# Optimization experiments

Measured on AMD Instinct MI355X. Metric: run time of the kernel, lower is better.

Reference implementation:

```python
import jax, jax.numpy as jnp
import numpy as np

N = 4096      # nodes
D = 256       # input_dim
OUT = 256     # output_dim
K = 4         # num_kernels
TOPK = 16
CHEB_T = 2
ROW_TEMP = 1.0
EPS = 1e-9


def setup_inputs() -> dict:
    key = jax.random.key(0)
    ks = jax.random.split(key, 6)
    X = jax.random.normal(ks[0], (N, D), dtype=jnp.float32)
    L_k = jax.random.normal(ks[1], (K, D, D), dtype=jnp.float32) * 0.02
    alpha = jnp.ones((K,), dtype=jnp.float32)
    theta = jax.random.normal(ks[2], (CHEB_T + 1, D), dtype=jnp.float32) * 0.02
    rho_raw = jnp.zeros((), dtype=jnp.float32)
    proj_w = jax.random.normal(ks[3], (OUT, D), dtype=jnp.float32) / np.float32(np.sqrt(D))
    proj_b = jnp.zeros((OUT,), dtype=jnp.float32)
    v0 = jax.random.normal(ks[4], (N, 1), dtype=jnp.float32)  # power-iteration init
    return dict(X=X, L_k=L_k, alpha=alpha, theta=theta, rho_raw=rho_raw,
                proj_w=proj_w, proj_b=proj_b, v0=v0)


def reference(X, L_k, alpha, theta, rho_raw, proj_w, proj_b, v0):
    n, d = X.shape
    k = L_k.shape[0]
    # 1) kernel stack: A_k = X L_k X^T / sqrt(D), row softmax  -> (K,N,N)
    A = jnp.einsum('nd,kde,me->knm', X, L_k, X) / jnp.sqrt(jnp.float32(d))
    H_stack = jax.nn.softmax(A / max(ROW_TEMP, 1e-6), axis=-1)
    w = jax.nn.softmax(alpha)[:, None, None]
    H_fused = (H_stack * w).sum(0)                               # (N,N)
    # 2) soft incidence via per-row top-k + renormalize, scattered into B (N, K*N)
    vals, idx = jax.lax.top_k(H_stack, TOPK)                     # (K,N,TOPK)
    vals = vals / (vals.sum(-1, keepdims=True) + EPS)
    E = k * n
    cols = jnp.arange(k)[:, None, None] * n + jnp.arange(n)[None, :, None]
    cols = jnp.broadcast_to(cols, idx.shape)
    B = jnp.zeros((n, E), X.dtype).at[idx.reshape(-1), cols.reshape(-1)].set(vals.reshape(-1))
    W = jnp.ones((E,), X.dtype)
    # 3) hypergraph Laplacian L = I - Dv^{-1/2} B W De^{-1} B^T Dv^{-1/2}
    De = B.sum(0) + EPS
    Dv = (B * W[None, :]).sum(1) + EPS
    Dv_is = 1.0 / jnp.sqrt(Dv)
    S = (B * (W / De)[None, :]) @ B.T                            # (N,N)
    S_norm = Dv_is[:, None] * S * Dv_is[None, :]
    L = jnp.eye(n, dtype=X.dtype) - S_norm
    # 4) lambda_max via power iteration on detached L (constant, as in torch)
    Ld = jax.lax.stop_gradient(L)
    v = v0 / (jnp.linalg.norm(v0) + EPS)
    for _ in range(5):
        v = Ld @ v
        v = v / (jnp.linalg.norm(v) + EPS)
    lam = jnp.maximum((v.T @ (Ld @ v)).squeeze(), jnp.float32(1e-3))
    lam = jax.lax.stop_gradient(lam)
    # Chebyshev filter
    L_tilde = (2.0 / lam) * L - jnp.eye(n, dtype=X.dtype)
    out = X * theta[0][None, :]
    T0 = X
    T1 = L_tilde @ X
    out = out + T1 * theta[1][None, :]
    for t in range(2, CHEB_T + 1):
        T2 = 2.0 * (L_tilde @ T1) - T0
        out = out + T2 * theta[t][None, :]
        T0, T1 = T1, T2
    Z_spec = jax.nn.elu(out)
    # 5) residual blend with kernel diffusion
    Z_kern = H_fused @ X
    rho = jax.nn.sigmoid(rho_raw)
    Z_mix = rho * Z_spec + (1.0 - rho) * Z_kern
    # 6) final projection
    return Z_mix @ proj_w.T + proj_b[None, :]
```

## Files before the change

kernel.cpp:

```cpp
#include <hip/hip_runtime.h>
#include <math.h>

#define N_ 4096
#define D_ 256
#define K_ 4
#define TK_ 16
#define E_ (K_ * N_)
#define NENT_ (E_ * TK_)

typedef unsigned short u16;
typedef unsigned int u32;
typedef __attribute__((ext_vector_type(8))) short bf16x8;
typedef __attribute__((ext_vector_type(4))) float f32x4;

__device__ __forceinline__ u16 bf16_rne(float x) {
  u32 u = __float_as_uint(x);
  u32 r = u + 0x7FFFu + ((u >> 16) & 1u);
  return (u16)(r >> 16);
}


__global__ void scalars_kernel(const float* __restrict__ alpha,
                               const float* __restrict__ rho_raw,
                               float* __restrict__ scal) {
  if (threadIdx.x == 0) {
    float m = alpha[0];
    for (int k = 1; k < K_; ++k) m = fmaxf(m, alpha[k]);
    float e[K_]; float s = 0.f;
    for (int k = 0; k < K_; ++k) { e[k] = expf(alpha[k] - m); s += e[k]; }
    for (int k = 0; k < K_; ++k) scal[k] = e[k] / s;
    scal[4] = 1.0f / (1.0f + expf(-rho_raw[0]));
  }
}

__global__ void dvis_kernel(const float* __restrict__ DvAcc, float* __restrict__ Dvis) {
  int i = blockIdx.x * 256 + threadIdx.x;
  Dvis[i] = 1.0f / sqrtf(DvAcc[i] + 1e-9f);
}

__global__ void make_tkvd(const float* __restrict__ tkv, const int* __restrict__ tki,
                          const float* __restrict__ Dvis, float* __restrict__ tkvd) {
  int i = blockIdx.x * 256 + threadIdx.x;
  tkvd[i] = tkv[i] * Dvis[tki[i]];
}

__global__ void cvt_split4(const float* __restrict__ in, u16* __restrict__ hi,
                           u16* __restrict__ lo) {
  int i = (blockIdx.x * 256 + threadIdx.x) * 4;
  float4 v = *(const float4*)(in + i);
  u16 h0 = bf16_rne(v.x), h1 = bf16_rne(v.y), h2 = bf16_rne(v.z), h3 = bf16_rne(v.w);
  float f0 = __uint_as_float((u32)h0 << 16), f1 = __uint_as_float((u32)h1 << 16);
  float f2 = __uint_as_float((u32)h2 << 16), f3 = __uint_as_float((u32)h3 << 16);
  u16 l0 = bf16_rne(v.x - f0), l1 = bf16_rne(v.y - f1);
  u16 l2 = bf16_rne(v.z - f2), l3 = bf16_rne(v.w - f3);
  *(uint2*)(hi + i) = make_uint2((u32)h0 | ((u32)h1 << 16), (u32)h2 | ((u32)h3 << 16));
  *(uint2*)(lo + i) = make_uint2((u32)l0 | ((u32)l1 << 16), (u32)l2 | ((u32)l3 << 16));
}

__global__ __launch_bounds__(256) void transpose_split(const float* __restrict__ X,
                                                       u16* __restrict__ ht,
                                                       u16* __restrict__ lt) {
  __shared__ float tile[32][33];
  const int tx = threadIdx.x & 31, ty = threadIdx.x >> 5;
  const int d0 = blockIdx.x * 32, n0 = blockIdx.y * 32;
#pragma unroll
  for (int q = 0; q < 4; ++q)
    tile[ty + q * 8][tx] = X[(size_t)(n0 + ty + q * 8) * D_ + d0 + tx];
  __syncthreads();
#pragma unroll
  for (int q = 0; q < 4; ++q) {
    int dd = ty + q * 8;
    float v = tile[tx][dd];
    u16 h = bf16_rne(v);
    float hf = __uint_as_float((u32)h << 16);
    u16 l = bf16_rne(v - hf);
    ht[(size_t)(d0 + dd) * N_ + n0 + tx] = h;
    lt[(size_t)(d0 + dd) * N_ + n0 + tx] = l;
  }
}

__global__ __launch_bounds__(256) void gemm_nn64_split(const float* __restrict__ A,
                                                       const float* __restrict__ B,
                                                       u16* __restrict__ Ch,
                                                       u16* __restrict__ Cl,
                                                       int Kdim, int lda, int ldb, int ldc) {
  __shared__ float As[16][68];
  __shared__ float Bs[16][68];
  const int tid = threadIdx.x;
  const int bm = blockIdx.x * 64, bn = blockIdx.y * 64;
  const int lrA = tid >> 2, lcA = (tid & 3) * 4;
  const int rrB = tid >> 4, ccB = (tid & 15) * 4;
  const int tx = tid & 15, ty = tid >> 4;
  const float* Ap = A + (size_t)(bm + lrA) * lda + lcA;
  const float* Bp = B + (size_t)rrB * ldb + bn + ccB;
  float acc[4][4] = {};
  for (int k0 = 0; k0 < Kdim; k0 += 16) {
    float4 av = *(const float4*)(Ap + k0);
    float4 bv = *(const float4*)(Bp + (size_t)k0 * ldb);
    __syncthreads();
    As[lcA + 0][lrA] = av.x; As[lcA + 1][lrA] = av.y;
    As[lcA + 2][lrA] = av.z; As[lcA + 3][lrA] = av.w;
    *(float4*)&Bs[rrB][ccB] = bv;
    __syncthreads();
#pragma unroll
    for (int kk = 0; kk < 16; ++kk) {
      float a[4], b[4];
      *(float4*)a = *(const float4*)&As[kk][ty * 4];
      *(float4*)b = *(const float4*)&Bs[kk][tx * 4];
#pragma unroll
      for (int i = 0; i < 4; ++i)
#pragma unroll
        for (int j = 0; j < 4; ++j) acc[i][j] += a[i] * b[j];
    }
  }
#pragma unroll
  for (int i = 0; i < 4; ++i) {
    int row = bm + ty * 4 + i;
    u16 h[4], lo[4];
#pragma unroll
    for (int j = 0; j < 4; ++j) {
      h[j] = bf16_rne(acc[i][j]);
      lo[j] = bf16_rne(acc[i][j] - __uint_as_float((u32)h[j] << 16));
    }
    size_t base = (size_t)row * ldc + bn + tx * 4;
    *(uint2*)(Ch + base) = make_uint2((u32)h[0] | ((u32)h[1] << 16), (u32)h[2] | ((u32)h[3] << 16));
    *(uint2*)(Cl + base) = make_uint2((u32)lo[0] | ((u32)lo[1] << 16), (u32)lo[2] | ((u32)lo[3] << 16));
  }
}

__global__ __launch_bounds__(256) void gemm_nt64_bias(const float* __restrict__ A,
                                                      const float* __restrict__ B,
                                                      const float* __restrict__ bias,
                                                      float* __restrict__ C,
                                                      int Kdim, int lda, int ldb, int ldc) {
  __shared__ float As[16][68];
  __shared__ float Bs[16][68];
  const int tid = threadIdx.x;
  const int bm = blockIdx.x * 64, bn = blockIdx.y * 64;
  const int lr = tid >> 2, lc = (tid & 3) * 4;
  const int tx = tid & 15, ty = tid >> 4;
  const float* Ap = A + (size_t)(bm + lr) * lda + lc;
  const float* Bp = B + (size_t)(bn + lr) * ldb + lc;
  float acc[4][4] = {};
  for (int k0 = 0; k0 < Kdim; k0 += 16) {
    float4 av = *(const float4*)(Ap + k0);
    float4 bv = *(const float4*)(Bp + k0);
    __syncthreads();
    As[lc + 0][lr] = av.x; As[lc + 1][lr] = av.y; As[lc + 2][lr] = av.z; As[lc + 3][lr] = av.w;
    Bs[lc + 0][lr] = bv.x; Bs[lc + 1][lr] = bv.y; Bs[lc + 2][lr] = bv.z; Bs[lc + 3][lr] = bv.w;
    __syncthreads();
#pragma unroll
    for (int kk = 0; kk < 16; ++kk) {
      float a[4], b[4];
      *(float4*)a = *(const float4*)&As[kk][ty * 4];
      *(float4*)b = *(const float4*)&Bs[kk][tx * 4];
#pragma unroll
      for (int i = 0; i < 4; ++i)
#pragma unroll
        for (int j = 0; j < 4; ++j) acc[i][j] += a[i] * b[j];
    }
  }
#pragma unroll
  for (int i = 0; i < 4; ++i) {
    int row = bm + ty * 4 + i;
    float4 o;
    o.x = acc[i][0] + bias[bn + tx * 4 + 0];
    o.y = acc[i][1] + bias[bn + tx * 4 + 1];
    o.z = acc[i][2] + bias[bn + tx * 4 + 2];
    o.w = acc[i][3] + bias[bn + tx * 4 + 3];
    *(float4*)(C + (size_t)row * ldc + bn + tx * 4) = o;
  }
}


__global__ __launch_bounds__(256) void scores_mfma(const u16* __restrict__ Ahg,
                                                   const u16* __restrict__ Alg,
                                                   const u16* __restrict__ Bhg,
                                                   const u16* __restrict__ Blg,
                                                   float* __restrict__ C, float scale) {
  __shared__ char smem[65536];
  const int tid = threadIdx.x;
  const int bm = blockIdx.x * 128, bn = blockIdx.y * 128;
  const int w = tid >> 6, l = tid & 63;
  const int wr = (w >> 1) * 64, wc = (w & 1) * 64;
  const int srow = tid >> 3, scol = (tid & 7) * 8;
  const int lb = l & 15, lke = (l >> 4) * 8;
  const u16* bh0 = Bhg + (size_t)(bn + wc + 0  + lb) * D_ + lke;
  const u16* bh1 = Bhg + (size_t)(bn + wc + 16 + lb) * D_ + lke;
  const u16* bh2 = Bhg + (size_t)(bn + wc + 32 + lb) * D_ + lke;
  const u16* bh3 = Bhg + (size_t)(bn + wc + 48 + lb) * D_ + lke;
  const size_t dlo = (size_t)(Blg - Bhg);
  const int aoff[4] = {
    (srow + 0)  * 128 + ((scol * 2) ^ (((srow + 0)  & 7) << 4)),
    (srow + 32) * 128 + ((scol * 2) ^ (((srow + 32) & 7) << 4)),
    (srow + 64) * 128 + ((scol * 2) ^ (((srow + 64) & 7) << 4)),
    (srow + 96) * 128 + ((scol * 2) ^ (((srow + 96) & 7) << 4)) };
  f32x4 acc[4][4];
#pragma unroll
  for (int i = 0; i < 4; ++i)
#pragma unroll
    for (int j = 0; j < 4; ++j) { acc[i][j][0] = 0.f; acc[i][j][1] = 0.f; acc[i][j][2] = 0.f; acc[i][j][3] = 0.f; }

  uint4 ah[4], al[4];
#pragma unroll
  for (int ii = 0; ii < 4; ++ii) {
    int r = srow + ii * 32;
    ah[ii] = *(const uint4*)(Ahg + (size_t)(bm + r) * D_ + scol);
    al[ii] = *(const uint4*)(Alg + (size_t)(bm + r) * D_ + scol);
  }
  {
    char* bAh = smem; char* bAl = smem + 16384;
#pragma unroll
    for (int ii = 0; ii < 4; ++ii) {
      *(uint4*)(bAh + aoff[ii]) = ah[ii];
      *(uint4*)(bAl + aoff[ii]) = al[ii];
    }
  }
  __syncthreads();

  for (int c = 0; c < 4; ++c) {
    char* bAh = smem + ((c & 1) << 15);
    char* bAl = bAh + 16384;
    const bool hn = (c < 3);
    if (hn) {
      const int kn = (c + 1) * 64;
#pragma unroll
      for (int ii = 0; ii < 4; ++ii) {
        int r = srow + ii * 32;
        ah[ii] = *(const uint4*)(Ahg + (size_t)(bm + r) * D_ + kn + scol);
        al[ii] = *(const uint4*)(Alg + (size_t)(bm + r) * D_ + kn + scol);
      }
    }
#pragma unroll
    for (int kk = 0; kk < 2; ++kk) {
      const int kb = kk * 64 + ((l >> 4) << 4);
      const int ge = c * 64 + kk * 32;
      bf16x8 fbh[4], fbl[4];
      fbh[0] = *(const bf16x8*)(bh0 + ge); fbl[0] = *(const bf16x8*)(bh0 + dlo + ge);
      fbh[1] = *(const bf16x8*)(bh1 + ge); fbl[1] = *(const bf16x8*)(bh1 + dlo + ge);
      fbh[2] = *(const bf16x8*)(bh2 + ge); fbl[2] = *(const bf16x8*)(bh2 + dlo + ge);
      fbh[3] = *(const bf16x8*)(bh3 + ge); fbl[3] = *(const bf16x8*)(bh3 + dlo + ge);
#pragma unroll
      for (int i = 0; i < 4; ++i) {
        int ra = wr + i * 16 + lb;
        int oa = ra * 128 + (kb ^ ((ra & 7) << 4));
        bf16x8 fah = *(const bf16x8*)(bAh + oa);
        bf16x8 fal = *(const bf16x8*)(bAl + oa);
#pragma unroll
        for (int j = 0; j < 4; ++j) {
          acc[i][j] = __builtin_amdgcn_mfma_f32_16x16x32_bf16(fah, fbh[j], acc[i][j], 0, 0, 0);
          acc[i][j] = __builtin_amdgcn_mfma_f32_16x16x32_bf16(fah, fbl[j], acc[i][j], 0, 0, 0);
          acc[i][j] = __builtin_amdgcn_mfma_f32_16x16x32_bf16(fal, fbh[j], acc[i][j], 0, 0, 0);
        }
      }
    }
    if (hn) {
      char* nAh = smem + (((c + 1) & 1) << 15);
      char* nAl = nAh + 16384;
#pragma unroll
      for (int ii = 0; ii < 4; ++ii) {
        *(uint4*)(nAh + aoff[ii]) = ah[ii];
        *(uint4*)(nAl + aoff[ii]) = al[ii];
      }
    }
    __syncthreads();
  }
  float* Cs = (float*)smem;
  const int cr = (l >> 4) * 4, cc = l & 15;
#pragma unroll
  for (int p = 0; p < 2; ++p) {
    __syncthreads();
    if ((w >> 1) == p) {
#pragma unroll
      for (int i = 0; i < 4; ++i)
#pragma unroll
        for (int r = 0; r < 4; ++r) {
          int rl = i * 16 + cr + r;
          int sw = ((rl >> 2) & 3) << 4;
#pragma unroll
          for (int j = 0; j < 4; ++j) {
            int cl = wc + j * 16 + cc;
            Cs[rl * 128 + (cl ^ sw)] = acc[i][j][r] * scale;
          }
        }
    }
    __syncthreads();
#pragma unroll
    for (int ii = 0; ii < 8; ++ii) {
      int rl = ii * 8 + (tid >> 5);
      int c4 = (tid & 31) * 4;
      float4 v = *(float4*)&Cs[rl * 128 + (c4 ^ (((rl >> 2) & 3) << 4))];
      *(float4*)(C + (size_t)(bm + p * 64 + rl) * N_ + bn + c4) = v;
    }
  }
}

__global__ __launch_bounds__(256) void zkern_mfma(const float* __restrict__ S,
                                                  const float* __restrict__ rowmax,
                                                  const float* __restrict__ rowZ,
                                                  const u16* __restrict__ BhT,
                                                  const u16* __restrict__ BlT,
                                                  float* __restrict__ Zpart,
                                                  const float* __restrict__ scal,
                                                  int kidx, int kchunk) {
  __shared__ char smem[32768];
  const int tid = threadIdx.x;
  const int bm = blockIdx.x * 128, bn = blockIdx.y * 128;
  const int kz = blockIdx.z;
  const int w = tid >> 6, l = tid & 63;
  const int wr = (w >> 1) * 64, wc = (w & 1) * 64;
  const int arow = tid >> 4, acol = (tid & 15) * 4;
  const int lb = l & 15, lke = (l >> 4) * 8;
  const u16* bh0 = BhT + (size_t)(bn + wc + 0  + lb) * N_ + lke;
  const u16* bh1 = BhT + (size_t)(bn + wc + 16 + lb) * N_ + lke;
  const u16* bh2 = BhT + (size_t)(bn + wc + 32 + lb) * N_ + lke;
  const u16* bh3 = BhT + (size_t)(bn + wc + 48 + lb) * N_ + lke;
  const size_t dlo = (size_t)(BlT - BhT);
  float rm[8];
  int aoff[8];
#pragma unroll
  for (int ii = 0; ii < 8; ++ii) {
    int r = arow + ii * 16;
    rm[ii] = rowmax[bm + r];
    aoff[ii] = r * 128 + ((acol * 2) ^ ((r & 7) << 4));
  }
  f32x4 acc[4][4];
#pragma unroll
  for (int i = 0; i < 4; ++i)
#pragma unroll
    for (int j = 0; j < 4; ++j) { acc[i][j][0] = 0.f; acc[i][j][1] = 0.f; acc[i][j][2] = 0.f; acc[i][j][3] = 0.f; }

  const int nchunk = kchunk >> 6;
  const int kbase = kz * kchunk;

  float4 sv[8];
#pragma unroll
  for (int ii = 0; ii < 8; ++ii)
    sv[ii] = *(const float4*)(S + (size_t)(bm + arow + ii * 16) * N_ + kbase + acol);
  {
    char* bAh = smem;
#pragma unroll
    for (int ii = 0; ii < 8; ++ii) {
      float e0 = expf(sv[ii].x - rm[ii]), e1 = expf(sv[ii].y - rm[ii]);
      float e2 = expf(sv[ii].z - rm[ii]), e3 = expf(sv[ii].w - rm[ii]);
      u16 h0 = bf16_rne(e0), h1 = bf16_rne(e1), h2 = bf16_rne(e2), h3 = bf16_rne(e3);
      *(uint2*)(bAh + aoff[ii]) = make_uint2((u32)h0 | ((u32)h1 << 16), (u32)h2 | ((u32)h3 << 16));
    }
  }
  __syncthreads();

  for (int c = 0; c < nchunk; ++c) {
    char* bAh = smem + ((c & 1) << 14);
    const bool hn = (c + 1 < nchunk);
    if (hn) {
      const int kn = kbase + (c + 1) * 64;
#pragma unroll
      for (int ii = 0; ii < 8; ++ii)
        sv[ii] = *(const float4*)(S + (size_t)(bm + arow + ii * 16) * N_ + kn + acol);
    }
#pragma unroll
    for (int kk = 0; kk < 2; ++kk) {
      const int kb = kk * 64 + ((l >> 4) << 4);
      const int ge = kbase + c * 64 + kk * 32;
      bf16x8 fbh[4], fbl[4];
      fbh[0] = *(const bf16x8*)(bh0 + ge); fbl[0] = *(const bf16x8*)(bh0 + dlo + ge);
      fbh[1] = *(const bf16x8*)(bh1 + ge); fbl[1] = *(const bf16x8*)(bh1 + dlo + ge);
      fbh[2] = *(const bf16x8*)(bh2 + ge); fbl[2] = *(const bf16x8*)(bh2 + dlo + ge);
      fbh[3] = *(const bf16x8*)(bh3 + ge); fbl[3] = *(const bf16x8*)(bh3 + dlo + ge);
#pragma unroll
      for (int i = 0; i < 4; ++i) {
        int ra = wr + i * 16 + lb;
        int oa = ra * 128 + (kb ^ ((ra & 7) << 4));
        bf16x8 fah = *(const bf16x8*)(bAh + oa);
#pragma unroll
        for (int j = 0; j < 4; ++j) {
          acc[i][j] = __builtin_amdgcn_mfma_f32_16x16x32_bf16(fah, fbh[j], acc[i][j], 0, 0, 0);
          acc[i][j] = __builtin_amdgcn_mfma_f32_16x16x32_bf16(fah, fbl[j], acc[i][j], 0, 0, 0);
        }
      }
    }
    if (hn) {
      char* nAh = smem + (((c + 1) & 1) << 14);
#pragma unroll
      for (int ii = 0; ii < 8; ++ii) {
        float e0 = expf(sv[ii].x - rm[ii]), e1 = expf(sv[ii].y - rm[ii]);
        float e2 = expf(sv[ii].z - rm[ii]), e3 = expf(sv[ii].w - rm[ii]);
        u16 h0 = bf16_rne(e0), h1 = bf16_rne(e1), h2 = bf16_rne(e2), h3 = bf16_rne(e3);
        *(uint2*)(nAh + aoff[ii]) = make_uint2((u32)h0 | ((u32)h1 << 16), (u32)h2 | ((u32)h3 << 16));
      }
    }
    __syncthreads();
  }
  const float wk = scal[kidx];
  float* Zp = Zpart + (size_t)kz * N_ * D_;
  float* Cs = (float*)smem;
  const int cr = (l >> 4) * 4, cc = l & 15;
#pragma unroll
  for (int p = 0; p < 2; ++p) {
    __syncthreads();
    if ((w >> 1) == p) {
#pragma unroll
      for (int i = 0; i < 4; ++i)
#pragma unroll
        for (int r = 0; r < 4; ++r) {
          int rl = i * 16 + cr + r;
          int sw = ((rl >> 2) & 3) << 4;
#pragma unroll
          for (int j = 0; j < 4; ++j) {
            int cl = wc + j * 16 + cc;
            Cs[rl * 128 + (cl ^ sw)] = acc[i][j][r];
          }
        }
    }
    __syncthreads();
#pragma unroll
    for (int ii = 0; ii < 8; ++ii) {
      int rl = ii * 8 + (tid >> 5);
      int c4 = (tid & 31) * 4;
      int row = bm + p * 64 + rl;
      float sc = wk / rowZ[row];
      float4 v = *(float4*)&Cs[rl * 128 + (c4 ^ (((rl >> 2) & 3) << 4))];
      float* zb = Zp + (size_t)row * D_ + bn + c4;
      float4 z = *(float4*)zb;
      z.x += sc * v.x; z.y += sc * v.y; z.z += sc * v.z; z.w += sc * v.w;
      *(float4*)zb = z;
    }
  }
}

__global__ __launch_bounds__(256) void rowstats_topk(const float* __restrict__ S,
                                                     float* __restrict__ rowmax,
                                                     float* __restrict__ rowZ,
                                                     float* __restrict__ tkv,
                                                     int* __restrict__ tki) {
  const int row = blockIdx.x, tid = threadIdx.x;
  const int wid = tid >> 6, lane = tid & 63;
  __shared__ int hist[1024];
  __shared__ int P[256];
  __shared__ float cval[256];
  __shared__ int cgi[256];
  __shared__ int ccnt;
  __shared__ int binlo_s;
  __shared__ float rv[4];
  __shared__ float stk[TK_];
  __shared__ int itk[TK_];
  __shared__ float tv16[TK_];
  __shared__ float mzs[3];

  hist[tid] = 0; hist[tid + 256] = 0; hist[tid + 512] = 0; hist[tid + 768] = 0;
  if (tid == 0) ccnt = 0;

  const float4* Sp = (const float4*)(S + (size_t)row * N_);
  float r[16];
  float lmax = -3.4e38f;
#pragma unroll
  for (int it = 0; it < 4; ++it) {
    float4 v = Sp[tid + it * 256];
    r[it * 4 + 0] = v.x; r[it * 4 + 1] = v.y; r[it * 4 + 2] = v.z; r[it * 4 + 3] = v.w;
    lmax = fmaxf(lmax, fmaxf(fmaxf(v.x, v.y), fmaxf(v.z, v.w)));
  }
#pragma unroll
  for (int off = 32; off; off >>= 1) lmax = fmaxf(lmax, __shfl_xor(lmax, off));
  if (lane == 0) rv[wid] = lmax;
  __syncthreads();
  if (tid == 0) mzs[0] = fmaxf(fmaxf(rv[0], rv[1]), fmaxf(rv[2], rv[3]));
  __syncthreads();
  const float M = mzs[0];
  float ls = 0.f;
#pragma unroll
  for (int j = 0; j < 16; ++j) ls += expf(r[j] - M);
#pragma unroll
  for (int off = 32; off; off >>= 1) ls += __shfl_xor(ls, off);
  if (lane == 0) rv[wid] = ls;
  __syncthreads();
  if (tid == 0) {
    float z = rv[0] + rv[1] + rv[2] + rv[3];
    mzs[1] = z; rowmax[row] = M; rowZ[row] = z;
  }
  __syncthreads();
  const float Z = mzs[1];

#pragma unroll
  for (int j = 0; j < 16; ++j) {
    u32 u = __float_as_uint(r[j]);
    u32 key = (u >> 31) ? ~u : (u | 0x80000000u);
    atomicAdd(&hist[key >> 22], 1);
  }
  __syncthreads();
  const int b0 = tid * 4;
  const int h0 = hist[b0], h1 = hist[b0 + 1], h2 = hist[b0 + 2], h3 = hist[b0 + 3];
  P[tid] = h0 + h1 + h2 + h3;
  __syncthreads();
  for (int o = 1; o < 256; o <<= 1) {
    int v = P[tid] + ((tid + o < 256) ? P[tid + o] : 0);
    __syncthreads();
    P[tid] = v;
    __syncthreads();
  }
  {
    int above = (tid < 255) ? P[tid + 1] : 0;
    int s3 = above + h3, s2 = s3 + h2, s1 = s2 + h1, s0 = s1 + h0;
    if (s3 >= TK_ && above < TK_) binlo_s = b0 + 3;
    else if (s2 >= TK_ && s3 < TK_) binlo_s = b0 + 2;
    else if (s1 >= TK_ && s2 < TK_) binlo_s = b0 + 1;
    else if (s0 >= TK_ && s1 < TK_) binlo_s = b0;
  }
  __syncthreads();
  const u32 kmin = (u32)binlo_s << 22;
#pragma unroll
  for (int j = 0; j < 16; ++j) {
    u32 u = __float_as_uint(r[j]);
    u32 key = (u >> 31) ? ~u : (u | 0x80000000u);
    if (key >= kmin) {
      int p = atomicAdd(&ccnt, 1);
      if (p < 256) {
        cval[p] = r[j];
        cgi[p] = 4 * tid + ((j >> 2) << 10) + (j & 3);
      }
    }
  }
  __syncthreads();
  const int nc = min(ccnt, 256);
  for (int t = 0; t < TK_; ++t) {
    if (tid < 64) {
      float bv = -3.4e38f; int bg = 0x7fffffff, bp = -1;
      for (int p = tid; p < nc; p += 64) {
        float v = cval[p]; int g = cgi[p];
        if (v > bv || (v == bv && g < bg)) { bv = v; bg = g; bp = p; }
      }
#pragma unroll
      for (int off = 32; off; off >>= 1) {
        float ov = __shfl_xor(bv, off);
        int og = __shfl_xor(bg, off);
        int op = __shfl_xor(bp, off);
        if (ov > bv || (ov == bv && og < bg)) { bv = ov; bg = og; bp = op; }
      }
      if (tid == 0) { stk[t] = bv; itk[t] = bg; cval[bp] = -3.4e38f; }
    }
    __syncthreads();
  }
  if (tid < TK_) tv16[tid] = expf(stk[tid] - M) / Z;
  __syncthreads();
  if (tid == 0) { float s = 0.f; for (int q = 0; q < TK_; ++q) s += tv16[q]; mzs[2] = s + 1e-9f; }
  __syncthreads();
  if (tid < TK_) {
    tkv[(size_t)row * TK_ + tid] = tv16[tid] / mzs[2];
    tki[(size_t)row * TK_ + tid] = itk[tid];
  }
}

__global__ void edge_scan(const float* __restrict__ tkv, const int* __restrict__ tki,
                          float* __restrict__ DvAcc, int* __restrict__ cnt,
                          float* __restrict__ invDe) {
  int e = blockIdx.x * 256 + threadIdx.x;
  float s = 0.f;
#pragma unroll
  for (int q = 0; q < TK_; ++q) s += tkv[(size_t)e * TK_ + q];
  invDe[e] = 1.0f / (s + 1e-9f);
#pragma unroll
  for (int q = 0; q < TK_; ++q) {
    int m = tki[(size_t)e * TK_ + q];
    atomicAdd(&DvAcc[m], tkv[(size_t)e * TK_ + q]);
    atomicAdd(&cnt[m], 1);
  }
}

__global__ __launch_bounds__(1024) void scan_offsets(const int* __restrict__ cnt,
                                                     int* __restrict__ off,
                                                     int* __restrict__ cur) {
  __shared__ int part[1024];
  const int t = threadIdx.x;
  const int b = t * 4;
  int c0 = cnt[b], c1 = cnt[b + 1], c2 = cnt[b + 2], c3 = cnt[b + 3];
  part[t] = c0 + c1 + c2 + c3;
  __syncthreads();
  for (int o = 1; o < 1024; o <<= 1) {
    int v = part[t] + ((t >= o) ? part[t - o] : 0);
    __syncthreads();
    part[t] = v;
    __syncthreads();
  }
  int ex = (t == 0) ? 0 : part[t - 1];
  off[b] = ex; off[b + 1] = ex + c0; off[b + 2] = ex + c0 + c1; off[b + 3] = ex + c0 + c1 + c2;
  cur[b] = off[b]; cur[b + 1] = off[b + 1]; cur[b + 2] = off[b + 2]; cur[b + 3] = off[b + 3];
  if (t == 1023) off[N_] = part[1023];
}

__global__ void edge_fill(const float* __restrict__ tkv, const int* __restrict__ tki,
                          int* __restrict__ cur, int* __restrict__ ince,
                          float* __restrict__ incv) {
  int e = blockIdx.x * 256 + threadIdx.x;
#pragma unroll
  for (int q = 0; q < TK_; ++q) {
    int m = tki[(size_t)e * TK_ + q];
    int pos = atomicAdd(&cur[m], 1);
    ince[pos] = e;
    incv[pos] = tkv[(size_t)e * TK_ + q];
  }
}

__global__ void pi_ye(const float* __restrict__ v, const float* __restrict__ tkvd,
                      const int* __restrict__ tki, const float* __restrict__ invDe,
                      float* __restrict__ ye) {
  int e = blockIdx.x * 256 + threadIdx.x;
  const float* tv = tkvd + (size_t)e * TK_;
  const int* ti = tki + (size_t)e * TK_;
  float a = 0.f;
#pragma unroll
  for (int q = 0; q < TK_; ++q) a += tv[q] * v[ti[q]];
  ye[e] = a * invDe[e];
}

__global__ void pi_step(const float* __restrict__ v, const float* __restrict__ ye,
                        const int* __restrict__ off, const int* __restrict__ ince,
                        const float* __restrict__ incv, const float* __restrict__ Dvis,
                        float* __restrict__ vn) {
  int m = blockIdx.x * 256 + threadIdx.x;
  float z = 0.f;
  int j0 = off[m], j1 = off[m + 1];
  for (int j = j0; j < j1; ++j) z += incv[j] * ye[ince[j]];
  vn[m] = v[m] - Dvis[m] * z;
}

__global__ __launch_bounds__(256) void pi_final(const float* __restrict__ v,
                                                const float* __restrict__ ye,
                                                const int* __restrict__ off,
                                                const int* __restrict__ ince,
                                                const float* __restrict__ incv,
                                                const float* __restrict__ Dvis,
                                                float* __restrict__ partial) {
  __shared__ float r1[256], r2[256];
  int m = blockIdx.x * 256 + threadIdx.x;
  float z = 0.f;
  int j0 = off[m], j1 = off[m + 1];
  for (int j = j0; j < j1; ++j) z += incv[j] * ye[ince[j]];
  float wv = v[m] - Dvis[m] * z;
  r1[threadIdx.x] = v[m] * wv;
  r2[threadIdx.x] = v[m] * v[m];
  __syncthreads();
  for (int s = 128; s; s >>= 1) {
    if (threadIdx.x < s) { r1[threadIdx.x] += r1[threadIdx.x + s]; r2[threadIdx.x] += r2[threadIdx.x + s]; }
    __syncthreads();
  }
  if (threadIdx.x == 0) { partial[blockIdx.x * 2] = r1[0]; partial[blockIdx.x * 2 + 1] = r2[0]; }
}

__global__ void pi_lam(const float* __restrict__ partial, float* __restrict__ scal) {
  if (threadIdx.x == 0) {
    float s1 = 0.f, s2 = 0.f;
    for (int b = 0; b < N_ / 256; ++b) { s1 += partial[2 * b]; s2 += partial[2 * b + 1]; }
    scal[5] = fmaxf(s1 / s2, 1e-3f);
  }
}

__global__ __launch_bounds__(256) void ye_mat(const float* __restrict__ M,
                                              const float* __restrict__ tkvd,
                                              const int* __restrict__ tki,
                                              const float* __restrict__ invDe,
                                              float* __restrict__ Ye) {
  const int w = threadIdx.x >> 6, l = threadIdx.x & 63;
  const int e = blockIdx.x * 4 + w;
  const float* tv = tkvd + (size_t)e * TK_;
  const int* ti = tki + (size_t)e * TK_;
  float4 a = make_float4(0.f, 0.f, 0.f, 0.f);
#pragma unroll
  for (int q = 0; q < TK_; ++q) {
    float v = tv[q];
    const float4 x = *(const float4*)(M + (size_t)ti[q] * D_ + l * 4);
    a.x += v * x.x; a.y += v * x.y; a.z += v * x.z; a.w += v * x.w;
  }
  const float s = invDe[e];
  float4 o; o.x = a.x * s; o.y = a.y * s; o.z = a.z * s; o.w = a.w * s;
  *(float4*)(Ye + (size_t)e * D_ + l * 4) = o;
}

__global__ __launch_bounds__(256) void bgather_combine(const float* __restrict__ Ye,
                                                       const int* __restrict__ off,
                                                       const int* __restrict__ ince,
                                                       const float* __restrict__ incv,
                                                       const float* __restrict__ Dvis,
                                                       const float* __restrict__ Mx,
                                                       const float* __restrict__ G,
                                                       const float* __restrict__ scal,
                                                       float* __restrict__ out, int mode) {
  const int w = threadIdx.x >> 6, l = threadIdx.x & 63;
  const int m = blockIdx.x * 4 + w;
  const int j0 = off[m], j1 = off[m + 1];
  float4 z = make_float4(0.f, 0.f, 0.f, 0.f);
  int j = j0;
  for (; j + 2 <= j1; j += 2) {
    float v0 = incv[j];     int e0 = ince[j];
    float v1 = incv[j + 1]; int e1 = ince[j + 1];
    float4 y0 = *(const float4*)(Ye + (size_t)e0 * D_ + l * 4);
    float4 y1 = *(const float4*)(Ye + (size_t)e1 * D_ + l * 4);
    z.x += v0 * y0.x + v1 * y1.x;
    z.y += v0 * y0.y + v1 * y1.y;
    z.z += v0 * y0.z + v1 * y1.z;
    z.w += v0 * y0.w + v1 * y1.w;
  }
  if (j < j1) {
    float v0 = incv[j]; int e0 = ince[j];
    float4 y0 = *(const float4*)(Ye + (size_t)e0 * D_ + l * 4);
    z.x += v0 * y0.x; z.y += v0 * y0.y; z.z += v0 * y0.z; z.w += v0 * y0.w;
  }
  const float lam = scal[5];
  const float c = 2.0f / lam;
  const float dv = Dvis[m];
  const size_t idx = (size_t)m * D_ + l * 4;
  float4 mx = *(const float4*)(Mx + idx);
  float4 o;
  if (mode == 1) {
    o.x = (c - 1.0f) * mx.x - c * dv * z.x;
    o.y = (c - 1.0f) * mx.y - c * dv * z.y;
    o.z = (c - 1.0f) * mx.z - c * dv * z.z;
    o.w = (c - 1.0f) * mx.w - c * dv * z.w;
  } else {
    float4 g = *(const float4*)(G + idx);
    o.x = (2.0f * c - 2.0f) * mx.x - 2.0f * c * dv * z.x - g.x;
    o.y = (2.0f * c - 2.0f) * mx.y - 2.0f * c * dv * z.y - g.y;
    o.z = (2.0f * c - 2.0f) * mx.z - 2.0f * c * dv * z.z - g.z;
    o.w = (2.0f * c - 2.0f) * mx.w - 2.0f * c * dv * z.w - g.w;
  }
  *(float4*)(out + idx) = o;
}

__global__ void mix_kernel(const float* __restrict__ X, const float* __restrict__ T1,
                           const float* __restrict__ T2, const float* __restrict__ theta,
                           const float* __restrict__ Zpart, int splitk,
                           const float* __restrict__ scal, float* __restrict__ Zmix) {
  const int i = blockIdx.x * 256 + threadIdx.x;
  const int d = i & (D_ - 1);
  float cheb = X[i] * theta[d] + T1[i] * theta[D_ + d] + T2[i] * theta[2 * D_ + d];
  float zs = cheb > 0.f ? cheb : expm1f(cheb);
  float zk = 0.f;
  for (int s = 0; s < splitk; ++s) zk += Zpart[(size_t)s * N_ * D_ + i];
  const float rho = scal[4];
  Zmix[i] = rho * zs + (1.0f - rho) * zk;
}


extern "C" void kernel_launch(void* const* d_in, const int* in_sizes, int n_in,
                              void* d_out, int out_size, void* d_ws, size_t ws_size,
                              hipStream_t stream) {
  const float* X       = (const float*)d_in[0];
  const float* L_k     = (const float*)d_in[1];
  const float* alpha   = (const float*)d_in[2];
  const float* theta   = (const float*)d_in[3];
  const float* rho_raw = (const float*)d_in[4];
  const float* proj_w  = (const float*)d_in[5];
  const float* proj_b  = (const float*)d_in[6];
  const float* v0      = (const float*)d_in[7];
  float* out = (float*)d_out;

  char* w = (char*)d_ws;
  size_t o = 0;
  auto alloc = [&](size_t bytes) -> char* {
    char* p = w + o; o += (bytes + 255) & ~(size_t)255; return p;
  };
  float* S     = (float*)alloc((size_t)N_ * N_ * 4);
  u16*   Xh    = (u16*)  alloc((size_t)N_ * D_ * 2);
  u16*   Xl    = (u16*)  alloc((size_t)N_ * D_ * 2);
  u16*   XhT   = (u16*)  alloc((size_t)D_ * N_ * 2);
  u16*   XlT   = (u16*)  alloc((size_t)D_ * N_ * 2);
  u16*   XLh   = (u16*)  alloc((size_t)N_ * D_ * 2);
  u16*   XLl   = (u16*)  alloc((size_t)N_ * D_ * 2);
  float* rowmax= (float*)alloc(N_ * 4);
  float* rowZ  = (float*)alloc(N_ * 4);
  float* tkv   = (float*)alloc((size_t)NENT_ * 4);
  int*   tki   = (int*)  alloc((size_t)NENT_ * 4);
  float* tkvd  = (float*)alloc((size_t)NENT_ * 4);
  float* invDe = (float*)alloc(E_ * 4);
  float* DvAcc = (float*)alloc(N_ * 4);
  float* Dvis  = (float*)alloc(N_ * 4);
  int*   cnt   = (int*)  alloc(N_ * 4);
  int*   off   = (int*)  alloc((N_ + 1) * 4);
  int*   cur   = (int*)  alloc(N_ * 4);
  int*   ince  = (int*)  alloc((size_t)NENT_ * 4);
  float* incv  = (float*)alloc((size_t)NENT_ * 4);
  float* va    = (float*)alloc(N_ * 4);
  float* vbuf  = (float*)alloc(N_ * 4);
  float* yev   = (float*)alloc(E_ * 4);
  float* part  = (float*)alloc((N_ / 256) * 2 * 4);
  float* scal  = (float*)alloc(256);
  int SPLITK = 8;
  while (SPLITK > 1 && o + (size_t)SPLITK * N_ * D_ * 4 > ws_size) SPLITK >>= 1;
  float* Zpart = (float*)alloc((size_t)SPLITK * N_ * D_ * 4);
  const int kchunk = N_ / SPLITK;
  float* Ye   = S + (size_t)N_ * D_;
  float* T1   = Ye + (size_t)E_ * D_;
  float* T2   = T1 + (size_t)N_ * D_;
  float* Zmix = T2 + (size_t)N_ * D_;

  scalars_kernel<<<1, 64, 0, stream>>>(alpha, rho_raw, scal);
  hipMemsetAsync(Zpart, 0, (size_t)SPLITK * N_ * D_ * 4, stream);
  hipMemsetAsync(DvAcc, 0, N_ * 4, stream);
  hipMemsetAsync(cnt, 0, N_ * 4, stream);

  cvt_split4<<<(N_ * D_ / 4) / 256, 256, 0, stream>>>(X, Xh, Xl);
  transpose_split<<<dim3(D_ / 32, N_ / 32), 256, 0, stream>>>(X, XhT, XlT);

  for (int k = 0; k < K_; ++k) {
    gemm_nn64_split<<<dim3(N_ / 64, D_ / 64), 256, 0, stream>>>(
        X, L_k + (size_t)k * D_ * D_, XLh, XLl, D_, D_, D_, D_);
    scores_mfma<<<dim3(N_ / 128, N_ / 128), 256, 0, stream>>>(
        XLh, XLl, Xh, Xl, S, 1.0f / 16.0f);
    rowstats_topk<<<N_, 256, 0, stream>>>(
        S, rowmax, rowZ, tkv + (size_t)k * N_ * TK_, tki + (size_t)k * N_ * TK_);
    zkern_mfma<<<dim3(N_ / 128, D_ / 128, SPLITK), 256, 0, stream>>>(
        S, rowmax, rowZ, XhT, XlT, Zpart, scal, k, kchunk);
  }

  edge_scan<<<E_ / 256, 256, 0, stream>>>(tkv, tki, DvAcc, cnt, invDe);
  dvis_kernel<<<N_ / 256, 256, 0, stream>>>(DvAcc, Dvis);
  make_tkvd<<<NENT_ / 256, 256, 0, stream>>>(tkv, tki, Dvis, tkvd);
  scan_offsets<<<1, 1024, 0, stream>>>(cnt, off, cur);
  edge_fill<<<E_ / 256, 256, 0, stream>>>(tkv, tki, cur, ince, incv);

  const float* vc = v0;
  float* vn = va;
  for (int it = 0; it < 5; ++it) {
    pi_ye<<<E_ / 256, 256, 0, stream>>>(vc, tkvd, tki, invDe, yev);
    pi_step<<<N_ / 256, 256, 0, stream>>>(vc, yev, off, ince, incv, Dvis, vn);
    vc = vn;
    vn = (vc == va) ? vbuf : va;
  }
  pi_ye<<<E_ / 256, 256, 0, stream>>>(vc, tkvd, tki, invDe, yev);
  pi_final<<<N_ / 256, 256, 0, stream>>>(vc, yev, off, ince, incv, Dvis, part);
  pi_lam<<<1, 64, 0, stream>>>(part, scal);

  ye_mat<<<E_ / 4, 256, 0, stream>>>(X, tkvd, tki, invDe, Ye);
  bgather_combine<<<N_ / 4, 256, 0, stream>>>(Ye, off, ince, incv, Dvis, X, X, scal, T1, 1);
  ye_mat<<<E_ / 4, 256, 0, stream>>>(T1, tkvd, tki, invDe, Ye);
  bgather_combine<<<N_ / 4, 256, 0, stream>>>(Ye, off, ince, incv, Dvis, T1, X, scal, T2, 2);

  mix_kernel<<<N_ * D_ / 256, 256, 0, stream>>>(X, T1, T2, theta, Zpart, SPLITK, scal, Zmix);

  gemm_nt64_bias<<<dim3(N_ / 64, D_ / 64), 256, 0, stream>>>(
      Zmix, proj_w, proj_b, out, D_, D_, D_, D_);
}
```

Baseline: 1.191 ms.

## Precompute bf16 exp scores in rowstats, replace histogram top-k with per-wave selection

The row-statistics kernel now writes exp(S - rowmax) as bf16 into a new N×N buffer. The diffusion GEMM then reads half-width data and skips its own exponentials. The histogram/candidate top-k is replaced by per-wave iterative argmax over registers followed by a merge of the per-wave top-16 lists. The split-K Zpart memset is dropped by having the first kernel pass overwrite instead of accumulate. The cost is an extra 32 MB write per kernel and a serial selection loop with 16 shuffle reductions per wave.

```diff
diff --git a/kernel.cpp b/kernel.cpp
--- a/kernel.cpp
+++ b/kernel.cpp
@@ -295,34 +295,31 @@
   }
 }
 
-__global__ __launch_bounds__(256) void zkern_mfma(const float* __restrict__ S,
-                                                  const float* __restrict__ rowmax,
+__global__ __launch_bounds__(256) void zkern_mfma(const u16* __restrict__ Hb,
                                                   const float* __restrict__ rowZ,
                                                   const u16* __restrict__ BhT,
                                                   const u16* __restrict__ BlT,
                                                   float* __restrict__ Zpart,
                                                   const float* __restrict__ scal,
-                                                  int kidx, int kchunk) {
+                                                  int kidx, int kchunk, int accum) {
   __shared__ char smem[32768];
   const int tid = threadIdx.x;
   const int bm = blockIdx.x * 128, bn = blockIdx.y * 128;
   const int kz = blockIdx.z;
   const int w = tid >> 6, l = tid & 63;
   const int wr = (w >> 1) * 64, wc = (w & 1) * 64;
-  const int arow = tid >> 4, acol = (tid & 15) * 4;
+  const int hrow = tid >> 4, hcol = (tid & 15) * 4;
   const int lb = l & 15, lke = (l >> 4) * 8;
   const u16* bh0 = BhT + (size_t)(bn + wc + 0  + lb) * N_ + lke;
   const u16* bh1 = BhT + (size_t)(bn + wc + 16 + lb) * N_ + lke;
   const u16* bh2 = BhT + (size_t)(bn + wc + 32 + lb) * N_ + lke;
   const u16* bh3 = BhT + (size_t)(bn + wc + 48 + lb) * N_ + lke;
   const size_t dlo = (size_t)(BlT - BhT);
-  float rm[8];
   int aoff[8];
 #pragma unroll
   for (int ii = 0; ii < 8; ++ii) {
-    int r = arow + ii * 16;
-    rm[ii] = rowmax[bm + r];
-    aoff[ii] = r * 128 + ((acol * 2) ^ ((r & 7) << 4));
+    int r = hrow + ii * 16;
+    aoff[ii] = r * 128 + ((hcol * 2) ^ ((r & 7) << 4));
   }
   f32x4 acc[4][4];
 #pragma unroll
@@ -333,19 +330,14 @@
   const int nchunk = kchunk >> 6;
   const int kbase = kz * kchunk;
 
-  float4 sv[8];
+  uint2 hv[8];
 #pragma unroll
   for (int ii = 0; ii < 8; ++ii)
-    sv[ii] = *(const float4*)(S + (size_t)(bm + arow + ii * 16) * N_ + kbase + acol);
+    hv[ii] = *(const uint2*)(Hb + (size_t)(bm + hrow + ii * 16) * N_ + kbase + hcol);
   {
     char* bAh = smem;
 #pragma unroll
-    for (int ii = 0; ii < 8; ++ii) {
-      float e0 = expf(sv[ii].x - rm[ii]), e1 = expf(sv[ii].y - rm[ii]);
-      float e2 = expf(sv[ii].z - rm[ii]), e3 = expf(sv[ii].w - rm[ii]);
-      u16 h0 = bf16_rne(e0), h1 = bf16_rne(e1), h2 = bf16_rne(e2), h3 = bf16_rne(e3);
-      *(uint2*)(bAh + aoff[ii]) = make_uint2((u32)h0 | ((u32)h1 << 16), (u32)h2 | ((u32)h3 << 16));
-    }
+    for (int ii = 0; ii < 8; ++ii) *(uint2*)(bAh + aoff[ii]) = hv[ii];
   }
   __syncthreads();
 
@@ -356,7 +348,7 @@
       const int kn = kbase + (c + 1) * 64;
 #pragma unroll
       for (int ii = 0; ii < 8; ++ii)
-        sv[ii] = *(const float4*)(S + (size_t)(bm + arow + ii * 16) * N_ + kn + acol);
+        hv[ii] = *(const uint2*)(Hb + (size_t)(bm + hrow + ii * 16) * N_ + kn + hcol);
     }
 #pragma unroll
     for (int kk = 0; kk < 2; ++kk) {
@@ -382,12 +374,7 @@
     if (hn) {
       char* nAh = smem + (((c + 1) & 1) << 14);
 #pragma unroll
-      for (int ii = 0; ii < 8; ++ii) {
-        float e0 = expf(sv[ii].x - rm[ii]), e1 = expf(sv[ii].y - rm[ii]);
-        float e2 = expf(sv[ii].z - rm[ii]), e3 = expf(sv[ii].w - rm[ii]);
-        u16 h0 = bf16_rne(e0), h1 = bf16_rne(e1), h2 = bf16_rne(e2), h3 = bf16_rne(e3);
-        *(uint2*)(nAh + aoff[ii]) = make_uint2((u32)h0 | ((u32)h1 << 16), (u32)h2 | ((u32)h3 << 16));
-      }
+      for (int ii = 0; ii < 8; ++ii) *(uint2*)(nAh + aoff[ii]) = hv[ii];
     }
     __syncthreads();
   }
@@ -421,9 +408,15 @@
       float sc = wk / rowZ[row];
       float4 v = *(float4*)&Cs[rl * 128 + (c4 ^ (((rl >> 2) & 3) << 4))];
       float* zb = Zp + (size_t)row * D_ + bn + c4;
-      float4 z = *(float4*)zb;
-      z.x += sc * v.x; z.y += sc * v.y; z.z += sc * v.z; z.w += sc * v.w;
-      *(float4*)zb = z;
+      if (accum) {
+        float4 z = *(float4*)zb;
+        z.x += sc * v.x; z.y += sc * v.y; z.z += sc * v.z; z.w += sc * v.w;
+        *(float4*)zb = z;
+      } else {
+        float4 z;
+        z.x = sc * v.x; z.y = sc * v.y; z.z = sc * v.z; z.w = sc * v.w;
+        *(float4*)zb = z;
+      }
     }
   }
 }
@@ -431,25 +424,19 @@
 __global__ __launch_bounds__(256) void rowstats_topk(const float* __restrict__ S,
                                                      float* __restrict__ rowmax,
                                                      float* __restrict__ rowZ,
+                                                     u16* __restrict__ Hb,
                                                      float* __restrict__ tkv,
                                                      int* __restrict__ tki) {
   const int row = blockIdx.x, tid = threadIdx.x;
   const int wid = tid >> 6, lane = tid & 63;
-  __shared__ int hist[1024];
-  __shared__ int P[256];
-  __shared__ float cval[256];
-  __shared__ int cgi[256];
-  __shared__ int ccnt;
-  __shared__ int binlo_s;
   __shared__ float rv[4];
+  __shared__ float wlv[4][TK_];
+  __shared__ int wli[4][TK_];
   __shared__ float stk[TK_];
   __shared__ int itk[TK_];
   __shared__ float tv16[TK_];
   __shared__ float mzs[3];
 
-  hist[tid] = 0; hist[tid + 256] = 0; hist[tid + 512] = 0; hist[tid + 768] = 0;
-  if (tid == 0) ccnt = 0;
-
   const float4* Sp = (const float4*)(S + (size_t)row * N_);
   float r[16];
   float lmax = -3.4e38f;
@@ -466,9 +453,10 @@
   if (tid == 0) mzs[0] = fmaxf(fmaxf(rv[0], rv[1]), fmaxf(rv[2], rv[3]));
   __syncthreads();
   const float M = mzs[0];
+  float eh[16];
   float ls = 0.f;
 #pragma unroll
-  for (int j = 0; j < 16; ++j) ls += expf(r[j] - M);
+  for (int j = 0; j < 16; ++j) { eh[j] = expf(r[j] - M); ls += eh[j]; }
 #pragma unroll
   for (int off = 32; off; off >>= 1) ls += __shfl_xor(ls, off);
   if (lane == 0) rv[wid] = ls;
@@ -477,68 +465,53 @@
     float z = rv[0] + rv[1] + rv[2] + rv[3];
     mzs[1] = z; rowmax[row] = M; rowZ[row] = z;
   }
+  u16* Hrow = Hb + (size_t)row * N_;
+#pragma unroll
+  for (int it = 0; it < 4; ++it) {
+    u16 h0 = bf16_rne(eh[it * 4 + 0]), h1 = bf16_rne(eh[it * 4 + 1]);
+    u16 h2 = bf16_rne(eh[it * 4 + 2]), h3 = bf16_rne(eh[it * 4 + 3]);
+    *(uint2*)(Hrow + it * 1024 + tid * 4) =
+        make_uint2((u32)h0 | ((u32)h1 << 16), (u32)h2 | ((u32)h3 << 16));
+  }
   __syncthreads();
   const float Z = mzs[1];
 
-#pragma unroll
-  for (int j = 0; j < 16; ++j) {
-    u32 u = __float_as_uint(r[j]);
-    u32 key = (u >> 31) ? ~u : (u | 0x80000000u);
-    atomicAdd(&hist[key >> 22], 1);
-  }
-  __syncthreads();
-  const int b0 = tid * 4;
-  const int h0 = hist[b0], h1 = hist[b0 + 1], h2 = hist[b0 + 2], h3 = hist[b0 + 3];
-  P[tid] = h0 + h1 + h2 + h3;
-  __syncthreads();
-  for (int o = 1; o < 256; o <<= 1) {
-    int v = P[tid] + ((tid + o < 256) ? P[tid + o] : 0);
-    __syncthreads();
-    P[tid] = v;
-    __syncthreads();
-  }
-  {
-    int above = (tid < 255) ? P[tid + 1] : 0;
-    int s3 = above + h3, s2 = s3 + h2, s1 = s2 + h1, s0 = s1 + h0;
-    if (s3 >= TK_ && above < TK_) binlo_s = b0 + 3;
-    else if (s2 >= TK_ && s3 < TK_) binlo_s = b0 + 2;
-    else if (s1 >= TK_ && s2 < TK_) binlo_s = b0 + 1;
-    else if (s0 >= TK_ && s1 < TK_) binlo_s = b0;
-  }
-  __syncthreads();
-  const u32 kmin = (u32)binlo_s << 22;
-#pragma unroll
-  for (int j = 0; j < 16; ++j) {
-    u32 u = __float_as_uint(r[j]);
-    u32 key = (u >> 31) ? ~u : (u | 0x80000000u);
-    if (key >= kmin) {
-      int p = atomicAdd(&ccnt, 1);
-      if (p < 256) {
-        cval[p] = r[j];
-        cgi[p] = 4 * tid + ((j >> 2) << 10) + (j & 3);
-      }
-    }
-  }
-  __syncthreads();
-  const int nc = min(ccnt, 256);
+  unsigned mask = 0;
   for (int t = 0; t < TK_; ++t) {
-    if (tid < 64) {
-      float bv = -3.4e38f; int bg = 0x7fffffff, bp = -1;
-      for (int p = tid; p < nc; p += 64) {
-        float v = cval[p]; int g = cgi[p];
-        if (v > bv || (v == bv && g < bg)) { bv = v; bg = g; bp = p; }
-      }
+    float bv = -3.4e38f; int bj = -1;
+#pragma unroll
+    for (int j = 0; j < 16; ++j) {
+      if (!(mask & (1u << j))) { float v = r[j]; if (v > bv) { bv = v; bj = j; } }
+    }
+    int gi = (bj < 0) ? 0x7fffffff : 4 * tid + ((bj >> 2) << 10) + (bj & 3);
+#pragma unroll
+    for (int off = 32; off; off >>= 1) {
+      float ov = __shfl_xor(bv, off);
+      int og = __shfl_xor(gi, off);
+      if (ov > bv || (ov == bv && og < gi)) { bv = ov; gi = og; }
+    }
+    if (lane == 0) { wlv[wid][t] = bv; wli[wid][t] = gi; }
+    if (((gi >> 2) & 255) == tid) mask |= 1u << (((gi >> 10) << 2) | (gi & 3));
+  }
+  __syncthreads();
+  if (wid == 0) {
+    float cv = wlv[lane >> 4][lane & 15];
+    int cg = wli[lane >> 4][lane & 15];
+    bool used = false;
+    for (int t = 0; t < TK_; ++t) {
+      float bv = used ? -3.4e38f : cv;
+      int bg = used ? 0x7fffffff : cg;
 #pragma unroll
       for (int off = 32; off; off >>= 1) {
         float ov = __shfl_xor(bv, off);
         int og = __shfl_xor(bg, off);
-        int op = __shfl_xor(bp, off);
-        if (ov > bv || (ov == bv && og < bg)) { bv = ov; bg = og; bp = op; }
+        if (ov > bv || (ov == bv && og < bg)) { bv = ov; bg = og; }
       }
-      if (tid == 0) { stk[t] = bv; itk[t] = bg; cval[bp] = -3.4e38f; }
-    }
-    __syncthreads();
-  }
+      if (lane == 0) { stk[t] = bv; itk[t] = bg; }
+      if (cg == bg) used = true;
+    }
+  }
+  __syncthreads();
   if (tid < TK_) tv16[tid] = expf(stk[tid] - M) / Z;
   __syncthreads();
   if (tid == 0) { float s = 0.f; for (int q = 0; q < TK_; ++q) s += tv16[q]; mzs[2] = s + 1e-9f; }
@@ -758,6 +731,7 @@
     char* p = w + o; o += (bytes + 255) & ~(size_t)255; return p;
   };
   float* S     = (float*)alloc((size_t)N_ * N_ * 4);
+  u16*   Hb    = (u16*)  alloc((size_t)N_ * N_ * 2);
   u16*   Xh    = (u16*)  alloc((size_t)N_ * D_ * 2);
   u16*   Xl    = (u16*)  alloc((size_t)N_ * D_ * 2);
   u16*   XhT   = (u16*)  alloc((size_t)D_ * N_ * 2);
@@ -792,7 +766,6 @@
   float* Zmix = T2 + (size_t)N_ * D_;
 
   scalars_kernel<<<1, 64, 0, stream>>>(alpha, rho_raw, scal);
-  hipMemsetAsync(Zpart, 0, (size_t)SPLITK * N_ * D_ * 4, stream);
   hipMemsetAsync(DvAcc, 0, N_ * 4, stream);
   hipMemsetAsync(cnt, 0, N_ * 4, stream);
 
@@ -805,9 +778,9 @@
     scores_mfma<<<dim3(N_ / 128, N_ / 128), 256, 0, stream>>>(
         XLh, XLl, Xh, Xl, S, 1.0f / 16.0f);
     rowstats_topk<<<N_, 256, 0, stream>>>(
-        S, rowmax, rowZ, tkv + (size_t)k * N_ * TK_, tki + (size_t)k * N_ * TK_);
+        S, rowmax, rowZ, Hb, tkv + (size_t)k * N_ * TK_, tki + (size_t)k * N_ * TK_);
     zkern_mfma<<<dim3(N_ / 128, D_ / 128, SPLITK), 256, 0, stream>>>(
-        S, rowmax, rowZ, XhT, XlT, Zpart, scal, k, kchunk);
+        Hb, rowZ, XhT, XlT, Zpart, scal, k, kchunk, (k > 0) ? 1 : 0);
   }
 
   edge_scan<<<E_ / 256, 256, 0, stream>>>(tkv, tki, DvAcc, cnt, invDe);
```

Result: slower. 1.294 ms (+8.6%).

## Precompute bf16 exp matrix in rowstats and drop Zpart memset

Applied to the files above, without the earlier changes.

rowstats_topk now writes exp(S - rowmax) as a bf16 matrix Hb while it computes the row sums. zkern_mfma reads that 2-byte matrix instead of re-reading fp32 S and recomputing expf, which halves its A-operand load traffic and removes exp work. The first kernel iteration overwrites Zpart instead of accumulating, so the separate memset is no longer needed. In exchange rowstats pays an extra N×N×2-byte write per kernel, and the workspace needs an extra 32 MB buffer.

```diff
diff --git a/kernel.cpp b/kernel.cpp
--- a/kernel.cpp
+++ b/kernel.cpp
@@ -295,34 +295,31 @@
   }
 }
 
-__global__ __launch_bounds__(256) void zkern_mfma(const float* __restrict__ S,
-                                                  const float* __restrict__ rowmax,
+__global__ __launch_bounds__(256) void zkern_mfma(const u16* __restrict__ Hb,
                                                   const float* __restrict__ rowZ,
                                                   const u16* __restrict__ BhT,
                                                   const u16* __restrict__ BlT,
                                                   float* __restrict__ Zpart,
                                                   const float* __restrict__ scal,
-                                                  int kidx, int kchunk) {
+                                                  int kidx, int kchunk, int accum) {
   __shared__ char smem[32768];
   const int tid = threadIdx.x;
   const int bm = blockIdx.x * 128, bn = blockIdx.y * 128;
   const int kz = blockIdx.z;
   const int w = tid >> 6, l = tid & 63;
   const int wr = (w >> 1) * 64, wc = (w & 1) * 64;
-  const int arow = tid >> 4, acol = (tid & 15) * 4;
+  const int hrow = tid >> 4, hcol = (tid & 15) * 4;
   const int lb = l & 15, lke = (l >> 4) * 8;
   const u16* bh0 = BhT + (size_t)(bn + wc + 0  + lb) * N_ + lke;
   const u16* bh1 = BhT + (size_t)(bn + wc + 16 + lb) * N_ + lke;
   const u16* bh2 = BhT + (size_t)(bn + wc + 32 + lb) * N_ + lke;
   const u16* bh3 = BhT + (size_t)(bn + wc + 48 + lb) * N_ + lke;
   const size_t dlo = (size_t)(BlT - BhT);
-  float rm[8];
   int aoff[8];
 #pragma unroll
   for (int ii = 0; ii < 8; ++ii) {
-    int r = arow + ii * 16;
-    rm[ii] = rowmax[bm + r];
-    aoff[ii] = r * 128 + ((acol * 2) ^ ((r & 7) << 4));
+    int r = hrow + ii * 16;
+    aoff[ii] = r * 128 + ((hcol * 2) ^ ((r & 7) << 4));
   }
   f32x4 acc[4][4];
 #pragma unroll
@@ -333,19 +330,14 @@
   const int nchunk = kchunk >> 6;
   const int kbase = kz * kchunk;
 
-  float4 sv[8];
+  uint2 hv[8];
 #pragma unroll
   for (int ii = 0; ii < 8; ++ii)
-    sv[ii] = *(const float4*)(S + (size_t)(bm + arow + ii * 16) * N_ + kbase + acol);
+    hv[ii] = *(const uint2*)(Hb + (size_t)(bm + hrow + ii * 16) * N_ + kbase + hcol);
   {
     char* bAh = smem;
 #pragma unroll
-    for (int ii = 0; ii < 8; ++ii) {
-      float e0 = expf(sv[ii].x - rm[ii]), e1 = expf(sv[ii].y - rm[ii]);
-      float e2 = expf(sv[ii].z - rm[ii]), e3 = expf(sv[ii].w - rm[ii]);
-      u16 h0 = bf16_rne(e0), h1 = bf16_rne(e1), h2 = bf16_rne(e2), h3 = bf16_rne(e3);
-      *(uint2*)(bAh + aoff[ii]) = make_uint2((u32)h0 | ((u32)h1 << 16), (u32)h2 | ((u32)h3 << 16));
-    }
+    for (int ii = 0; ii < 8; ++ii) *(uint2*)(bAh + aoff[ii]) = hv[ii];
   }
   __syncthreads();
 
@@ -356,7 +348,7 @@
       const int kn = kbase + (c + 1) * 64;
 #pragma unroll
       for (int ii = 0; ii < 8; ++ii)
-        sv[ii] = *(const float4*)(S + (size_t)(bm + arow + ii * 16) * N_ + kn + acol);
+        hv[ii] = *(const uint2*)(Hb + (size_t)(bm + hrow + ii * 16) * N_ + kn + hcol);
     }
 #pragma unroll
     for (int kk = 0; kk < 2; ++kk) {
@@ -382,12 +374,7 @@
     if (hn) {
       char* nAh = smem + (((c + 1) & 1) << 14);
 #pragma unroll
-      for (int ii = 0; ii < 8; ++ii) {
-        float e0 = expf(sv[ii].x - rm[ii]), e1 = expf(sv[ii].y - rm[ii]);
-        float e2 = expf(sv[ii].z - rm[ii]), e3 = expf(sv[ii].w - rm[ii]);
-        u16 h0 = bf16_rne(e0), h1 = bf16_rne(e1), h2 = bf16_rne(e2), h3 = bf16_rne(e3);
-        *(uint2*)(nAh + aoff[ii]) = make_uint2((u32)h0 | ((u32)h1 << 16), (u32)h2 | ((u32)h3 << 16));
-      }
+      for (int ii = 0; ii < 8; ++ii) *(uint2*)(nAh + aoff[ii]) = hv[ii];
     }
     __syncthreads();
   }
@@ -421,9 +408,15 @@
       float sc = wk / rowZ[row];
       float4 v = *(float4*)&Cs[rl * 128 + (c4 ^ (((rl >> 2) & 3) << 4))];
       float* zb = Zp + (size_t)row * D_ + bn + c4;
-      float4 z = *(float4*)zb;
-      z.x += sc * v.x; z.y += sc * v.y; z.z += sc * v.z; z.w += sc * v.w;
-      *(float4*)zb = z;
+      if (accum) {
+        float4 z = *(float4*)zb;
+        z.x += sc * v.x; z.y += sc * v.y; z.z += sc * v.z; z.w += sc * v.w;
+        *(float4*)zb = z;
+      } else {
+        float4 z;
+        z.x = sc * v.x; z.y = sc * v.y; z.z = sc * v.z; z.w = sc * v.w;
+        *(float4*)zb = z;
+      }
     }
   }
 }
@@ -431,6 +424,7 @@
 __global__ __launch_bounds__(256) void rowstats_topk(const float* __restrict__ S,
                                                      float* __restrict__ rowmax,
                                                      float* __restrict__ rowZ,
+                                                     u16* __restrict__ Hb,
                                                      float* __restrict__ tkv,
                                                      int* __restrict__ tki) {
   const int row = blockIdx.x, tid = threadIdx.x;
@@ -466,9 +460,10 @@
   if (tid == 0) mzs[0] = fmaxf(fmaxf(rv[0], rv[1]), fmaxf(rv[2], rv[3]));
   __syncthreads();
   const float M = mzs[0];
+  float eh[16];
   float ls = 0.f;
 #pragma unroll
-  for (int j = 0; j < 16; ++j) ls += expf(r[j] - M);
+  for (int j = 0; j < 16; ++j) { eh[j] = expf(r[j] - M); ls += eh[j]; }
 #pragma unroll
   for (int off = 32; off; off >>= 1) ls += __shfl_xor(ls, off);
   if (lane == 0) rv[wid] = ls;
@@ -476,6 +471,14 @@
   if (tid == 0) {
     float z = rv[0] + rv[1] + rv[2] + rv[3];
     mzs[1] = z; rowmax[row] = M; rowZ[row] = z;
+  }
+  u16* Hrow = Hb + (size_t)row * N_;
+#pragma unroll
+  for (int it = 0; it < 4; ++it) {
+    u16 h0 = bf16_rne(eh[it * 4 + 0]), h1 = bf16_rne(eh[it * 4 + 1]);
+    u16 h2 = bf16_rne(eh[it * 4 + 2]), h3 = bf16_rne(eh[it * 4 + 3]);
+    *(uint2*)(Hrow + it * 1024 + tid * 4) =
+        make_uint2((u32)h0 | ((u32)h1 << 16), (u32)h2 | ((u32)h3 << 16));
   }
   __syncthreads();
   const float Z = mzs[1];
@@ -758,6 +761,7 @@
     char* p = w + o; o += (bytes + 255) & ~(size_t)255; return p;
   };
   float* S     = (float*)alloc((size_t)N_ * N_ * 4);
+  u16*   Hb    = (u16*)  alloc((size_t)N_ * N_ * 2);
   u16*   Xh    = (u16*)  alloc((size_t)N_ * D_ * 2);
   u16*   Xl    = (u16*)  alloc((size_t)N_ * D_ * 2);
   u16*   XhT   = (u16*)  alloc((size_t)D_ * N_ * 2);
@@ -792,7 +796,6 @@
   float* Zmix = T2 + (size_t)N_ * D_;
 
   scalars_kernel<<<1, 64, 0, stream>>>(alpha, rho_raw, scal);
-  hipMemsetAsync(Zpart, 0, (size_t)SPLITK * N_ * D_ * 4, stream);
   hipMemsetAsync(DvAcc, 0, N_ * 4, stream);
   hipMemsetAsync(cnt, 0, N_ * 4, stream);
 
@@ -805,9 +808,9 @@
     scores_mfma<<<dim3(N_ / 128, N_ / 128), 256, 0, stream>>>(
         XLh, XLl, Xh, Xl, S, 1.0f / 16.0f);
     rowstats_topk<<<N_, 256, 0, stream>>>(
-        S, rowmax, rowZ, tkv + (size_t)k * N_ * TK_, tki + (size_t)k * N_ * TK_);
+        S, rowmax, rowZ, Hb, tkv + (size_t)k * N_ * TK_, tki + (size_t)k * N_ * TK_);
     zkern_mfma<<<dim3(N_ / 128, D_ / 128, SPLITK), 256, 0, stream>>>(
-        S, rowmax, rowZ, XhT, XlT, Zpart, scal, k, kchunk);
+        Hb, rowZ, XhT, XlT, Zpart, scal, k, kchunk, (k > 0) ? 1 : 0);
   }
 
   edge_scan<<<E_ / 256, 256, 0, stream>>>(tkv, tki, DvAcc, cnt, invDe);
```

Result: no change. 1.191 ms (+0.1%).
